# Kernel optimization log

Hardware: AMD Instinct MI355X
Metric: run time of the kernel (lower is better)

## Reference

```python
import jax, jax.numpy as jnp
import numpy as np

N = 20000
E = 320000
IN_CH = 512
OUT_CH = 256


def setup_inputs() -> dict:
    key = jax.random.key(0)
    ks = jax.random.split(key, 24)
    p = lambda k, shape: jax.random.normal(k, shape, jnp.float32) * 0.05
    return {
        "x": jax.random.normal(ks[0], (N, IN_CH), jnp.float32),
        "edge_index": jax.random.randint(ks[1], (2, E), 0, N),
        "original_size": 16384,
        "W1": p(ks[2], (IN_CH, 4 * 256)), "as1": p(ks[3], (4, 256)), "ad1": p(ks[4], (4, 256)), "b1": p(ks[5], (1024,)),
        "lw1": p(ks[6], (IN_CH, 1024)), "lb1": p(ks[7], (1024,)),
        "W2": p(ks[8], (1024, 4 * 256)), "as2": p(ks[9], (4, 256)), "ad2": p(ks[10], (4, 256)), "b2": p(ks[11], (1024,)),
        "lw2": p(ks[12], (1024, 1024)), "lb2": p(ks[13], (1024,)),
        "W3": p(ks[14], (1024, 6 * 256)), "as3": p(ks[15], (6, 256)), "ad3": p(ks[16], (6, 256)), "b3": p(ks[17], (256,)),
        "lw3": p(ks[18], (1024, OUT_CH)), "lb3": p(ks[19], (OUT_CH,)),
    }


def gat_conv(x, src, dst, W, a_src, a_dst, bias, heads, ch, concat):
    """PyG-style GATConv: gather -> edge attention -> segment softmax -> scatter-add."""
    n = x.shape[0]
    h = (x @ W).reshape(n, heads, ch)                      # [N,H,C]
    alpha_s = (h * a_src[None]).sum(-1)                    # [N,H]
    alpha_d = (h * a_dst[None]).sum(-1)                    # [N,H]
    e = jax.nn.leaky_relu(alpha_s[src] + alpha_d[dst], 0.2)  # [E,H]
    m = jax.ops.segment_max(e, dst, num_segments=n)        # per-dst max (stable softmax)
    e = jnp.exp(e - m[dst])
    denom = jax.ops.segment_sum(e, dst, num_segments=n)
    alpha = e / (denom[dst] + 1e-16)                       # [E,H]
    msg = h[src] * alpha[:, :, None]                       # [E,H,C]
    out = jax.ops.segment_sum(msg, dst, num_segments=n)    # [N,H,C]
    out = out.reshape(n, heads * ch) if concat else out.mean(axis=1)
    return out + bias


def reference(x, edge_index, original_size, W1, as1, ad1, b1, lw1, lb1,
              W2, as2, ad2, b2, lw2, lb2, W3, as3, ad3, b3, lw3, lb3):
    n = x.shape[0]
    loops = jnp.arange(n)
    src = jnp.concatenate([edge_index[0], loops])  # PyG add_self_loops=True default
    dst = jnp.concatenate([edge_index[1], loops])
    h = jax.nn.elu(gat_conv(x, src, dst, W1, as1, ad1, b1, 4, 256, True) + x @ lw1 + lb1)
    h = jax.nn.elu(gat_conv(h, src, dst, W2, as2, ad2, b2, 4, 256, True) + h @ lw2 + lb2)
    h = gat_conv(h, src, dst, W3, as3, ad3, b3, 6, 256, False) + h @ lw3 + lb3
    return h[:original_size]
```

## Files before the change

kernel.cpp:

```cpp
#include <hip/hip_runtime.h>

#define N_NODES 20000
#define M_PAD   20096
#define E_EDGES 320000

typedef unsigned short u16;
typedef unsigned int   u32;
typedef __attribute__((ext_vector_type(8))) short bf16x8;
typedef __attribute__((ext_vector_type(4))) float f32x4;
typedef __attribute__((ext_vector_type(4))) u32   u32x4;

__device__ __forceinline__ float bf2f(u16 u){
  u32 x = ((u32)u) << 16; float f; __builtin_memcpy(&f, &x, 4); return f;
}
__device__ __forceinline__ u16 f2bf(float f){
  u32 u; __builtin_memcpy(&u, &f, 4);
  u += 0x7fffu + ((u >> 16) & 1u);
  return (u16)(u >> 16);
}
__device__ __forceinline__ float lrelu(float x){ return x > 0.f ? x : 0.2f * x; }

__device__ __forceinline__ void gl_lds16(const void* g, void* l){
  __builtin_amdgcn_global_load_lds((const __attribute__((address_space(1))) void*)g,
                                   (__attribute__((address_space(3))) void*)l, 16, 0, 0);
}

__device__ __forceinline__ void acc8(float* acc, float w, u32x4 p){
#pragma unroll
  for (int d = 0; d < 4; d++){
    u32 u = p[d];
    acc[2 * d]     += w * bf2f((u16)(u & 0xffff));
    acc[2 * d + 1] += w * bf2f((u16)(u >> 16));
  }
}

__global__ void hist_k(const int* __restrict__ ei, int* __restrict__ cnt){
  int i = blockIdx.x * 256 + threadIdx.x;
  if (i < E_EDGES) atomicAdd(&cnt[ei[E_EDGES + i]], 1);
}

__global__ void scan_k(const int* __restrict__ cnt, int* __restrict__ rowp,
                       int* __restrict__ fill, int n){
  __shared__ int wsum[16], wpre[16];
  __shared__ int carry;
  int tid = threadIdx.x, lane = tid & 63, wv = tid >> 6;
  if (tid == 0) carry = 0;
  __syncthreads();
  for (int base = 0; base < n; base += 1024){
    int i = base + tid;
    int v = (i < n) ? cnt[i] : 0;
    int incl = v;
#pragma unroll
    for (int d = 1; d < 64; d <<= 1){
      int t = __shfl_up(incl, d, 64);
      if (lane >= d) incl += t;
    }
    if (lane == 63) wsum[wv] = incl;
    __syncthreads();
    if (tid == 0){
      int s = carry;
#pragma unroll
      for (int w = 0; w < 16; w++){ wpre[w] = s; s += wsum[w]; }
      carry = s;
    }
    __syncthreads();
    if (i < n){ int e = wpre[wv] + incl - v; rowp[i] = e; fill[i] = e; }
  }
  __syncthreads();
  if (tid == 0) rowp[n] = carry;
}

__global__ void scatter_k(const int* __restrict__ ei, int* __restrict__ fill, int* __restrict__ esrc){
  int i = blockIdx.x * 256 + threadIdx.x;
  if (i < E_EDGES){
    int d = ei[E_EDGES + i];
    int p = atomicAdd(&fill[d], 1);
    esrc[p] = ei[i];
  }
}

__global__ void tcast_all(const float* __restrict__ W1, const float* __restrict__ lw1, u16* __restrict__ Wt1,
                          const float* __restrict__ W2, const float* __restrict__ lw2, u16* __restrict__ Wt2,
                          const float* __restrict__ W3, const float* __restrict__ lw3, u16* __restrict__ Wt3)
{
  __shared__ float tile[32][33];
  int b = blockIdx.x;
  const float* src; u16* dst; int Nc, n0, ldd;
  if      (b <  512){            src = W1;  Nc = 1024; dst = Wt1; n0 = 0;    ldd = 512;  }
  else if (b < 1024){ b -=  512; src = lw1; Nc = 1024; dst = Wt1; n0 = 1024; ldd = 512;  }
  else if (b < 2048){ b -= 1024; src = W2;  Nc = 1024; dst = Wt2; n0 = 0;    ldd = 1024; }
  else if (b < 3072){ b -= 2048; src = lw2; Nc = 1024; dst = Wt2; n0 = 1024; ldd = 1024; }
  else if (b < 4608){ b -= 3072; src = W3;  Nc = 1536; dst = Wt3; n0 = 0;    ldd = 1024; }
  else              { b -= 4608; src = lw3; Nc = 256;  dst = Wt3; n0 = 1536; ldd = 1024; }
  int gx = Nc / 32;
  int kb = (b / gx) * 32, nb = (b % gx) * 32;
  int tx = threadIdx.x, ty = threadIdx.y;
#pragma unroll
  for (int r = 0; r < 32; r += 8)
    tile[ty + r][tx] = src[(size_t)(kb + ty + r) * Nc + nb + tx];
  __syncthreads();
#pragma unroll
  for (int r = 0; r < 32; r += 8){
    int n = nb + ty + r;
    dst[(size_t)(n0 + n) * ldd + kb + tx] = f2bf(tile[tx][ty + r]);
  }
}

__global__ void castx_k(const float* __restrict__ x, u16* __restrict__ o, int realRows){
  int r = blockIdx.x, c = threadIdx.x * 2;
  float2 v = (r < realRows) ? *(const float2*)(x + (size_t)r * 512 + c) : make_float2(0.f, 0.f);
  u32 pk = ((u32)f2bf(v.y) << 16) | (u32)f2bf(v.x);
  *(u32*)(o + (size_t)r * 512 + c) = pk;
}

__global__ void zpad_k(u16* __restrict__ p, int n){
  int i = blockIdx.x * 256 + threadIdx.x; if (i < n) p[i] = 0;
}

__global__ __launch_bounds__(256, 2)
void gemm_bf16(const u16* __restrict__ A, const u16* __restrict__ Bt, u16* __restrict__ C,
               int N, int K,
               const float* __restrict__ a_s, const float* __restrict__ a_d,
               float* __restrict__ aS, float* __restrict__ aD, int H)
{
  __shared__ __attribute__((aligned(16))) u16 lA[128 * 32];
  __shared__ __attribute__((aligned(16))) u16 lB[256 * 32];
  const int tid  = threadIdx.x;
  const int wave = tid >> 6, lane = tid & 63;
  const int bn = blockIdx.x, bm = blockIdx.y;
  const int wm = (wave >> 1) * 64, wn = (wave & 1) * 128;

  const int srow  = wave * 16 + (lane >> 2);
  const int skcol = (lane & 3) * 8;
  const u16* Ag0 = A  + (size_t)(bm * 128 + srow) * K + skcol;
  const u16* Ag1 = Ag0 + (size_t)64 * K;
  const u16* Bg  = Bt + (size_t)(bn * 256 + srow) * K + skcol;
  u16* lA0 = lA + wave * 512; u16* lA1 = lA + 2048 + wave * 512;
  u16* lBw = lB + wave * 512;

  f32x4 acc[4][8] = {};

  for (int k0 = 0; k0 < K; k0 += 32){
    gl_lds16(Ag0 + k0, lA0);
    gl_lds16(Ag1 + k0, lA1);
#pragma unroll
    for (int c = 0; c < 4; c++)
      gl_lds16(Bg + (size_t)(c * 64) * K + k0, lBw + c * 2048);
    __syncthreads();
    const int koff = (lane >> 4) * 8;
    const int rsel = lane & 15;
    bf16x8 af[4], bfr[8];
#pragma unroll
    for (int i = 0; i < 4; i++) af[i]  = *(const bf16x8*)&lA[(wm + i * 16 + rsel) * 32 + koff];
#pragma unroll
    for (int j = 0; j < 8; j++) bfr[j] = *(const bf16x8*)&lB[(wn + j * 16 + rsel) * 32 + koff];
#pragma unroll
    for (int i = 0; i < 4; i++)
#pragma unroll
      for (int j = 0; j < 8; j++)
        acc[i][j] = __builtin_amdgcn_mfma_f32_16x16x32_bf16(af[i], bfr[j], acc[i][j], 0, 0, 0);
    __syncthreads();
  }

  const int r0 = (lane >> 4) * 4, cl = lane & 15;
#pragma unroll
  for (int i = 0; i < 4; i++)
#pragma unroll
    for (int j = 0; j < 8; j++){
      int row = bm * 128 + wm + i * 16 + r0;
      int col = bn * 256 + wn + j * 16 + cl;
      u16* cp = C + (size_t)row * N + col;
#pragma unroll
      for (int r = 0; r < 4; r++) cp[(size_t)r * N] = f2bf(acc[i][j][r]);
    }

  if (bn < H){
    float* fa = (float*)lA;
    fa[tid]       = a_s[bn * 256 + tid];
    fa[256 + tid] = a_d[bn * 256 + tid];
    __syncthreads();
    float* fb = (float*)lB;
    const int q = lane >> 4;
#pragma unroll
    for (int i = 0; i < 4; i++)
#pragma unroll
      for (int r = 0; r < 4; r++){
        float ps = 0.f, pd = 0.f;
#pragma unroll
        for (int j = 0; j < 8; j++){
          float v = acc[i][j][r];
          int c = wn + j * 16 + cl;
          ps += v * fa[c];
          pd += v * fa[256 + c];
        }
#pragma unroll
        for (int m = 1; m < 16; m <<= 1){
          ps += __shfl_xor(ps, m, 64);
          pd += __shfl_xor(pd, m, 64);
        }
        if (cl == 0){
          int row = wm + i * 16 + q * 4 + r;
          fb[(wave & 1) * 128 + row]       = ps;
          fb[256 + (wave & 1) * 128 + row] = pd;
        }
      }
    __syncthreads();
    if (tid < 128){
      int row = bm * 128 + tid;
      aS[(size_t)row * 8 + bn] = fb[tid] + fb[128 + tid];
      aD[(size_t)row * 8 + bn] = fb[256 + tid] + fb[384 + tid];
    }
  }
}

__global__ __launch_bounds__(256)
void agg4w_k(const u16* __restrict__ HG, int ldH,
             const int* __restrict__ rowp, const int* __restrict__ esrc,
             const float* __restrict__ aS, const float* __restrict__ aD,
             const float* __restrict__ bias, const float* __restrict__ lbias,
             u16* __restrict__ outb)
{
  __shared__ float s_w[4][256];
  const int tid = threadIdx.x, lane = tid & 63, wv = tid >> 6;
  const int dst = blockIdx.x * 4 + wv;
  const int e0 = rowp[dst];
  const int deg = rowp[dst + 1] - e0;
  const int nE = deg + 1;
  const float4 adv = *(const float4*)(aD + (size_t)dst * 8);

  int myS = dst;
  float ea = -1e30f, eb = -1e30f, ec = -1e30f, ed = -1e30f;
  if (lane < nE){
    myS = (lane == deg) ? dst : esrc[e0 + lane];
    float4 as = *(const float4*)(aS + (size_t)myS * 8);
    ea = lrelu(as.x + adv.x); eb = lrelu(as.y + adv.y);
    ec = lrelu(as.z + adv.z); ed = lrelu(as.w + adv.w);
  }
  float m0 = ea, m1 = eb, m2 = ec, m3 = ed;
  for (int i = lane + 64; i < nE; i += 64){
    int s = (i == deg) ? dst : esrc[e0 + i];
    float4 as = *(const float4*)(aS + (size_t)s * 8);
    m0 = fmaxf(m0, lrelu(as.x + adv.x)); m1 = fmaxf(m1, lrelu(as.y + adv.y));
    m2 = fmaxf(m2, lrelu(as.z + adv.z)); m3 = fmaxf(m3, lrelu(as.w + adv.w));
  }
#pragma unroll
  for (int off = 1; off < 64; off <<= 1){
    m0 = fmaxf(m0, __shfl_xor(m0, off)); m1 = fmaxf(m1, __shfl_xor(m1, off));
    m2 = fmaxf(m2, __shfl_xor(m2, off)); m3 = fmaxf(m3, __shfl_xor(m3, off));
  }

  float w0 = __expf(ea - m0), w1 = __expf(eb - m1);
  float w2 = __expf(ec - m2), w3 = __expf(ed - m3);
  float l0 = w0, l1 = w1, l2 = w2, l3 = w3;
  for (int i = lane + 64; i < nE; i += 64){
    int s = (i == deg) ? dst : esrc[e0 + i];
    float4 as = *(const float4*)(aS + (size_t)s * 8);
    l0 += __expf(lrelu(as.x + adv.x) - m0); l1 += __expf(lrelu(as.y + adv.y) - m1);
    l2 += __expf(lrelu(as.z + adv.z) - m2); l3 += __expf(lrelu(as.w + adv.w) - m3);
  }
#pragma unroll
  for (int off = 1; off < 64; off <<= 1){
    l0 += __shfl_xor(l0, off); l1 += __shfl_xor(l1, off);
    l2 += __shfl_xor(l2, off); l3 += __shfl_xor(l3, off);
  }
  float d0 = 1.f / (l0 + 1e-16f), d1 = 1.f / (l1 + 1e-16f);
  float d2 = 1.f / (l2 + 1e-16f), d3 = 1.f / (l3 + 1e-16f);
  *(float4*)&s_w[wv][lane * 4] = make_float4(w0 * d0, w1 * d1, w2 * d2, w3 * d3);
  __syncthreads();

  const int h = lane >> 4;
  const int ch0 = lane * 16;
  const float mh   = (h < 2) ? (h == 0 ? m0 : m1) : (h == 2 ? m2 : m3);
  const float dh   = (h < 2) ? (h == 0 ? d0 : d1) : (h == 2 ? d2 : d3);
  const float advh = (h < 2) ? (h == 0 ? adv.x : adv.y) : (h == 2 ? adv.z : adv.w);
  float acc[16] = {};
  const u16* HGc = HG + ch0;
  const int nF = nE < 64 ? nE : 64;
  int i = 0;
  for (; i + 3 < nF; i += 4){
    int sA = __shfl(myS, i),     sB = __shfl(myS, i + 1);
    int sC = __shfl(myS, i + 2), sD = __shfl(myS, i + 3);
    float wA = s_w[wv][i * 4 + h],       wB = s_w[wv][(i + 1) * 4 + h];
    float wC = s_w[wv][(i + 2) * 4 + h], wD = s_w[wv][(i + 3) * 4 + h];
    const u16* ra = HGc + (size_t)sA * ldH;
    const u16* rb = HGc + (size_t)sB * ldH;
    const u16* rc = HGc + (size_t)sC * ldH;
    const u16* rd = HGc + (size_t)sD * ldH;
    u32x4 pa0 = *(const u32x4*)ra, pa1 = *(const u32x4*)(ra + 8);
    u32x4 pb0 = *(const u32x4*)rb, pb1 = *(const u32x4*)(rb + 8);
    u32x4 pc0 = *(const u32x4*)rc, pc1 = *(const u32x4*)(rc + 8);
    u32x4 pd0 = *(const u32x4*)rd, pd1 = *(const u32x4*)(rd + 8);
    acc8(acc, wA, pa0); acc8(acc + 8, wA, pa1);
    acc8(acc, wB, pb0); acc8(acc + 8, wB, pb1);
    acc8(acc, wC, pc0); acc8(acc + 8, wC, pc1);
    acc8(acc, wD, pd0); acc8(acc + 8, wD, pd1);
  }
  for (; i < nF; i++){
    int sA = __shfl(myS, i);
    float wA = s_w[wv][i * 4 + h];
    const u16* ra = HGc + (size_t)sA * ldH;
    acc8(acc, wA, *(const u32x4*)ra); acc8(acc + 8, wA, *(const u32x4*)(ra + 8));
  }
  for (int j = 64; j < nE; j++){
    int s = (j == deg) ? dst : esrc[e0 + j];
    float e = lrelu(aS[(size_t)s * 8 + h] + advh);
    float w = __expf(e - mh) * dh;
    const u16* r = HGc + (size_t)s * ldH;
    acc8(acc, w, *(const u32x4*)r); acc8(acc + 8, w, *(const u32x4*)(r + 8));
  }

  const u16* lr = HG + (size_t)dst * ldH + 1024 + ch0;
  u32x4 q0 = *(const u32x4*)lr, q1 = *(const u32x4*)(lr + 8);
  float lin[16];
#pragma unroll
  for (int d = 0; d < 4; d++){
    lin[2*d]     = bf2f((u16)(q0[d] & 0xffff)); lin[2*d+1]   = bf2f((u16)(q0[d] >> 16));
    lin[8+2*d]   = bf2f((u16)(q1[d] & 0xffff)); lin[8+2*d+1] = bf2f((u16)(q1[d] >> 16));
  }
  u32 o[8];
#pragma unroll
  for (int d = 0; d < 8; d++){
    float va = acc[2*d]   + bias[ch0 + 2*d]   + lin[2*d]   + lbias[ch0 + 2*d];
    float vb = acc[2*d+1] + bias[ch0 + 2*d+1] + lin[2*d+1] + lbias[ch0 + 2*d+1];
    va = va > 0.f ? va : __expf(va) - 1.f;
    vb = vb > 0.f ? vb : __expf(vb) - 1.f;
    o[d] = ((u32)f2bf(vb) << 16) | (u32)f2bf(va);
  }
  u16* op = outb + (size_t)dst * 1024 + ch0;
  *(u32x4*)op = *(u32x4*)o;
  *(u32x4*)(op + 8) = *(u32x4*)(o + 4);
}

__global__ __launch_bounds__(256)
void agg6w_k(const u16* __restrict__ HG, int ldH,
             const int* __restrict__ rowp, const int* __restrict__ esrc,
             const float* __restrict__ aS, const float* __restrict__ aD,
             const float* __restrict__ bias, const float* __restrict__ lbias,
             float* __restrict__ outf)
{
  __shared__ float s_w[4][64 * 6];
  const int tid = threadIdx.x, lane = tid & 63, wv = tid >> 6;
  const int dst = blockIdx.x * 4 + wv;
  const int e0 = rowp[dst];
  const int deg = rowp[dst + 1] - e0;
  const int nE = deg + 1;

  const float* advp = aD + (size_t)dst * 8;
  float4 av4 = *(const float4*)advp; float2 av2 = *(const float2*)(advp + 4);
  float adv[6] = { av4.x, av4.y, av4.z, av4.w, av2.x, av2.y };

  int myS = dst;
  float e[6];
#pragma unroll
  for (int h = 0; h < 6; h++) e[h] = -1e30f;
  if (lane < nE){
    myS = (lane == deg) ? dst : esrc[e0 + lane];
    float4 a0 = *(const float4*)(aS + (size_t)myS * 8);
    float2 a1 = *(const float2*)(aS + (size_t)myS * 8 + 4);
    e[0] = lrelu(a0.x + adv[0]); e[1] = lrelu(a0.y + adv[1]);
    e[2] = lrelu(a0.z + adv[2]); e[3] = lrelu(a0.w + adv[3]);
    e[4] = lrelu(a1.x + adv[4]); e[5] = lrelu(a1.y + adv[5]);
  }
  float m[6];
#pragma unroll
  for (int h = 0; h < 6; h++) m[h] = e[h];
  for (int i = lane + 64; i < nE; i += 64){
    int s = (i == deg) ? dst : esrc[e0 + i];
    float4 a0 = *(const float4*)(aS + (size_t)s * 8);
    float2 a1 = *(const float2*)(aS + (size_t)s * 8 + 4);
    float t[6] = { a0.x, a0.y, a0.z, a0.w, a1.x, a1.y };
#pragma unroll
    for (int h = 0; h < 6; h++) m[h] = fmaxf(m[h], lrelu(t[h] + adv[h]));
  }
#pragma unroll
  for (int h = 0; h < 6; h++)
#pragma unroll
    for (int off = 1; off < 64; off <<= 1) m[h] = fmaxf(m[h], __shfl_xor(m[h], off));

  float w[6], l[6];
#pragma unroll
  for (int h = 0; h < 6; h++){ w[h] = __expf(e[h] - m[h]); l[h] = w[h]; }
  for (int i = lane + 64; i < nE; i += 64){
    int s = (i == deg) ? dst : esrc[e0 + i];
    float4 a0 = *(const float4*)(aS + (size_t)s * 8);
    float2 a1 = *(const float2*)(aS + (size_t)s * 8 + 4);
    float t[6] = { a0.x, a0.y, a0.z, a0.w, a1.x, a1.y };
#pragma unroll
    for (int h = 0; h < 6; h++) l[h] += __expf(lrelu(t[h] + adv[h]) - m[h]);
  }
#pragma unroll
  for (int h = 0; h < 6; h++)
#pragma unroll
    for (int off = 1; off < 64; off <<= 1) l[h] += __shfl_xor(l[h], off);
  float dv[6];
#pragma unroll
  for (int h = 0; h < 6; h++) dv[h] = (1.f / 6.f) / (l[h] + 1e-16f);
  float* swp = &s_w[wv][lane * 6];
  ((float2*)swp)[0] = make_float2(w[0] * dv[0], w[1] * dv[1]);
  ((float2*)swp)[1] = make_float2(w[2] * dv[2], w[3] * dv[3]);
  ((float2*)swp)[2] = make_float2(w[4] * dv[4], w[5] * dv[5]);
  __syncthreads();

  const int li = lane & 31, half = lane >> 5;
  const int ch0 = li * 8;
  float acc[8] = {};
  const u16* HGc = HG + ch0;
  const int nF = nE < 64 ? nE : 64;
  for (int i = half; i < nF; i += 2){
    int s = __shfl(myS, i);
    const u16* r = HGc + (size_t)s * ldH;
    const float* wp6 = &s_w[wv][i * 6];
#pragma unroll
    for (int h = 0; h < 6; h++){
      u32x4 p = *(const u32x4*)(r + h * 256);
      acc8(acc, wp6[h], p);
    }
  }
  for (int j = 64 + half; j < nE; j += 2){
    int s = (j == deg) ? dst : esrc[e0 + j];
    float4 a0 = *(const float4*)(aS + (size_t)s * 8);
    float2 a1 = *(const float2*)(aS + (size_t)s * 8 + 4);
    float t[6] = { a0.x, a0.y, a0.z, a0.w, a1.x, a1.y };
    const u16* r = HGc + (size_t)s * ldH;
#pragma unroll
    for (int h = 0; h < 6; h++){
      float wt = __expf(lrelu(t[h] + adv[h]) - m[h]) * dv[h];
      u32x4 p = *(const u32x4*)(r + h * 256);
      acc8(acc, wt, p);
    }
  }
#pragma unroll
  for (int c = 0; c < 8; c++) acc[c] += __shfl_xor(acc[c], 32);

  if (lane < 32){
    u32x4 q = *(const u32x4*)(HG + (size_t)dst * ldH + 1536 + ch0);
    float lin[8];
#pragma unroll
    for (int d = 0; d < 4; d++){
      lin[2*d]   = bf2f((u16)(q[d] & 0xffff));
      lin[2*d+1] = bf2f((u16)(q[d] >> 16));
    }
    float4 b0 = *(const float4*)(bias + ch0),  b1 = *(const float4*)(bias + ch0 + 4);
    float4 c0 = *(const float4*)(lbias + ch0), c1 = *(const float4*)(lbias + ch0 + 4);
    float4 o0, o1;
    o0.x = acc[0] + b0.x + lin[0] + c0.x; o0.y = acc[1] + b0.y + lin[1] + c0.y;
    o0.z = acc[2] + b0.z + lin[2] + c0.z; o0.w = acc[3] + b0.w + lin[3] + c0.w;
    o1.x = acc[4] + b1.x + lin[4] + c1.x; o1.y = acc[5] + b1.y + lin[5] + c1.y;
    o1.z = acc[6] + b1.z + lin[6] + c1.z; o1.w = acc[7] + b1.w + lin[7] + c1.w;
    float* op = outf + (size_t)dst * 256 + ch0;
    *(float4*)op = o0;
    *(float4*)(op + 4) = o1;
  }
}

extern "C" void kernel_launch(void* const* d_in, const int* in_sizes, int n_in,
                              void* d_out, int out_size, void* d_ws, size_t ws_size,
                              hipStream_t stream)
{
  const float* x   = (const float*)d_in[0];
  const int*   ei  = (const int*)  d_in[1];
  const float* W1  = (const float*)d_in[3];
  const float* as1 = (const float*)d_in[4];
  const float* ad1 = (const float*)d_in[5];
  const float* b1  = (const float*)d_in[6];
  const float* lw1 = (const float*)d_in[7];
  const float* lb1 = (const float*)d_in[8];
  const float* W2  = (const float*)d_in[9];
  const float* as2 = (const float*)d_in[10];
  const float* ad2 = (const float*)d_in[11];
  const float* b2  = (const float*)d_in[12];
  const float* lw2 = (const float*)d_in[13];
  const float* lb2 = (const float*)d_in[14];
  const float* W3  = (const float*)d_in[15];
  const float* as3 = (const float*)d_in[16];
  const float* ad3 = (const float*)d_in[17];
  const float* b3  = (const float*)d_in[18];
  const float* lw3 = (const float*)d_in[19];
  const float* lb3 = (const float*)d_in[20];

  char* wp = (char*)d_ws;
  auto nxt = [&](size_t b) -> void* {
    void* p = (void*)wp; wp += (b + 255) & ~(size_t)255; return p;
  };
  u16*  Wt1  = (u16*) nxt((size_t)2048 * 512  * 2);
  u16*  Wt2  = (u16*) nxt((size_t)2048 * 1024 * 2);
  u16*  Wt3  = (u16*) nxt((size_t)1792 * 1024 * 2);
  u16*  Xb   = (u16*) nxt((size_t)M_PAD * 1024 * 2);
  u16*  HG   = (u16*) nxt((size_t)M_PAD * 2048 * 2);
  float* aS  = (float*)nxt((size_t)M_PAD * 8 * 4);
  float* aD  = (float*)nxt((size_t)M_PAD * 8 * 4);
  int*  cnt  = (int*)  nxt((size_t)N_NODES * 4);
  int*  rowp = (int*)  nxt((size_t)(N_NODES + 1) * 4);
  int*  fill = (int*)  nxt((size_t)N_NODES * 4);
  int*  esrc = (int*)  nxt((size_t)E_EDGES * 4);

  hipMemsetAsync(cnt, 0, (size_t)N_NODES * 4, stream);
  hist_k   <<<(E_EDGES + 255) / 256, 256, 0, stream>>>(ei, cnt);
  scan_k   <<<1, 1024, 0, stream>>>(cnt, rowp, fill, N_NODES);
  scatter_k<<<(E_EDGES + 255) / 256, 256, 0, stream>>>(ei, fill, esrc);

  tcast_all<<<4864, dim3(32, 8), 0, stream>>>(W1, lw1, Wt1, W2, lw2, Wt2, W3, lw3, Wt3);

  castx_k<<<M_PAD, 256, 0, stream>>>(x, Xb, N_NODES);
  zpad_k <<<(96 * 1024 + 255) / 256, 256, 0, stream>>>(Xb + (size_t)N_NODES * 1024, 96 * 1024);

  const int MT = M_PAD / 128;

  gemm_bf16<<<dim3(2048 / 256, MT), 256, 0, stream>>>(Xb, Wt1, HG, 2048, 512,  as1, ad1, aS, aD, 4);
  agg4w_k  <<<N_NODES / 4, 256, 0, stream>>>(HG, 2048, rowp, esrc, aS, aD, b1, lb1, Xb);

  gemm_bf16<<<dim3(2048 / 256, MT), 256, 0, stream>>>(Xb, Wt2, HG, 2048, 1024, as2, ad2, aS, aD, 4);
  agg4w_k  <<<N_NODES / 4, 256, 0, stream>>>(HG, 2048, rowp, esrc, aS, aD, b2, lb2, Xb);

  gemm_bf16<<<dim3(1792 / 256, MT), 256, 0, stream>>>(Xb, Wt3, HG, 1792, 1024, as3, ad3, aS, aD, 6);
  int outRows = out_size / 256;
  agg6w_k  <<<outRows / 4, 256, 0, stream>>>(HG, 1792, rowp, esrc, aS, aD, b3, lb3, (float*)d_out);

  (void)in_sizes; (void)n_in; (void)ws_size;
}
```

Baseline: 840.9 us.

## Double-buffer LDS tiles in bf16 GEMM to overlap loads with MFMA

Merges the A and B shared-memory tiles into one ping-pong buffer pair. The first k-tile is prefetched before the loop, and each iteration issues the next tile's global-to-LDS loads before running the MFMAs on the current tile. One barrier per iteration replaces two. The aim is to hide global load latency behind matrix math, at the cost of doubling the LDS footprint (about 48KB per block), which may limit occupancy.

```diff
diff --git a/kernel.cpp b/kernel.cpp
--- a/kernel.cpp
+++ b/kernel.cpp
@@ -123,8 +123,7 @@
                const float* __restrict__ a_s, const float* __restrict__ a_d,
                float* __restrict__ aS, float* __restrict__ aD, int H)
 {
-  __shared__ __attribute__((aligned(16))) u16 lA[128 * 32];
-  __shared__ __attribute__((aligned(16))) u16 lB[256 * 32];
+  __shared__ __attribute__((aligned(16))) u16 lAB[2][12288];
   const int tid  = threadIdx.x;
   const int wave = tid >> 6, lane = tid & 63;
   const int bn = blockIdx.x, bm = blockIdx.y;
@@ -135,18 +134,36 @@
   const u16* Ag0 = A  + (size_t)(bm * 128 + srow) * K + skcol;
   const u16* Ag1 = Ag0 + (size_t)64 * K;
   const u16* Bg  = Bt + (size_t)(bn * 256 + srow) * K + skcol;
-  u16* lA0 = lA + wave * 512; u16* lA1 = lA + 2048 + wave * 512;
-  u16* lBw = lB + wave * 512;
+  const int woff = wave * 512;
 
   f32x4 acc[4][8] = {};
 
+  {
+    u16* a0 = &lAB[0][woff];
+    u16* a1 = &lAB[0][2048 + woff];
+    u16* bw = &lAB[0][4096 + woff];
+    gl_lds16(Ag0, a0);
+    gl_lds16(Ag1, a1);
+#pragma unroll
+    for (int c = 0; c < 4; c++)
+      gl_lds16(Bg + (size_t)(c * 64) * K, bw + c * 2048);
+  }
+
   for (int k0 = 0; k0 < K; k0 += 32){
-    gl_lds16(Ag0 + k0, lA0);
-    gl_lds16(Ag1 + k0, lA1);
-#pragma unroll
-    for (int c = 0; c < 4; c++)
-      gl_lds16(Bg + (size_t)(c * 64) * K + k0, lBw + c * 2048);
+    const int p = (k0 >> 5) & 1;
     __syncthreads();
+    if (k0 + 32 < K){
+      u16* a0 = &lAB[p ^ 1][woff];
+      u16* a1 = &lAB[p ^ 1][2048 + woff];
+      u16* bw = &lAB[p ^ 1][4096 + woff];
+      gl_lds16(Ag0 + k0 + 32, a0);
+      gl_lds16(Ag1 + k0 + 32, a1);
+#pragma unroll
+      for (int c = 0; c < 4; c++)
+        gl_lds16(Bg + (size_t)(c * 64) * K + k0 + 32, bw + c * 2048);
+    }
+    const u16* lA = &lAB[p][0];
+    const u16* lB = &lAB[p][4096];
     const int koff = (lane >> 4) * 8;
     const int rsel = lane & 15;
     bf16x8 af[4], bfr[8];
@@ -159,7 +176,6 @@
 #pragma unroll
       for (int j = 0; j < 8; j++)
         acc[i][j] = __builtin_amdgcn_mfma_f32_16x16x32_bf16(af[i], bfr[j], acc[i][j], 0, 0, 0);
-    __syncthreads();
   }
 
   const int r0 = (lane >> 4) * 4, cl = lane & 15;
@@ -175,11 +191,12 @@
     }
 
   if (bn < H){
-    float* fa = (float*)lA;
+    __syncthreads();
+    float* fa = (float*)&lAB[0][0];
     fa[tid]       = a_s[bn * 256 + tid];
     fa[256 + tid] = a_d[bn * 256 + tid];
     __syncthreads();
-    float* fb = (float*)lB;
+    float* fb = (float*)&lAB[1][0];
     const int q = lane >> 4;
 #pragma unroll
     for (int i = 0; i < 4; i++)
```

Result: faster. 804.2 us (-4.4%).
